# Kernel tuning notes

Measured on AMD Instinct MI355X. Metric: run time of the kernel, lower is better.

## Reference

```python
import jax, jax.numpy as jnp
from jax import lax
import numpy as np

BIG = 1234567891011.0  # sentinel used by the original DTW_TF


def _dtw_cost(D):
    """DTW cost matrix, D: [K,K] pairwise distances -> cost: [K+1,K+1]."""
    K = D.shape[0]
    prev = jnp.concatenate([jnp.zeros((1,), D.dtype), jnp.full((K,), BIG, D.dtype)])  # row 0

    def row_step(prev_row, d_row):
        def col_step(left, vals):
            d, diag, up = vals
            c = d + jnp.minimum(jnp.minimum(left, diag), up)
            return c, c
        _, row_tail = lax.scan(col_step, jnp.asarray(BIG, D.dtype), (d_row, prev_row[:-1], prev_row[1:]))
        row = jnp.concatenate([jnp.full((1,), BIG, D.dtype), row_tail])
        return row, row

    _, rows = lax.scan(row_step, prev, D)
    return jnp.concatenate([prev[None, :], rows], axis=0)


def _dwa_unit(S, W):
    """DTW-aligned 'trace' between window S [K,C] and filter W [K,C].
    Equals trace(gather(S,pi) @ gather(W,pw)^T) = sum over path of dot(S[pi],W[pw])."""
    K = S.shape[0]
    dots = S @ W.T  # [K,K], dots[i,j] = <S[i], W[j]>
    sq = jnp.sum(S * S, axis=1)[:, None] + jnp.sum(W * W, axis=1)[None, :] - 2.0 * dots
    D = jnp.sqrt(jnp.maximum(sq, 0.0))  # euclidean distance matrix
    cost = _dtw_cost(D)  # [K+1,K+1]

    # Backtrack minimal path from (K,K); path has at most 2K-1 kept entries.
    # Original writes (i-1,j-1) each loop iter then drops the last write; the
    # trace is order-independent so we accumulate kept dot-products directly.
    def step(carry, _):
        i, j, acc, active = carry
        cands = jnp.stack([cost[i - 1, j - 1], cost[i, j - 1], cost[i - 1, j]])
        m = jnp.argmin(cands)  # ties -> first, matching tf.argmin
        i2 = i - jnp.where(m == 1, 0, 1)
        j2 = j - jnp.where(m == 2, 0, 1)
        nxt = active & (i2 > 0) & (j2 > 0)  # loop continues -> this write is kept
        acc = acc + jnp.where(nxt, dots[i2 - 1, j2 - 1], 0.0)
        i = jnp.where(active, i2, i)
        j = jnp.where(active, j2, j)
        return (i, j, acc, nxt), None

    init = (jnp.int32(K), jnp.int32(K), dots[K - 1, K - 1], jnp.bool_(True))
    (_, _, acc, _), _ = lax.scan(step, init, None, length=2 * K - 1)
    return acc


def _dwa_cnn(x, w, b):
    K = w.shape[0]
    P = x.shape[1] - K + 1
    Wt = jnp.transpose(w, (2, 0, 1))  # [F,K,C]
    idx = jnp.arange(P)[:, None] + jnp.arange(K)[None, :]  # [P,K]
    windows = x[:, idx, :]  # [B,P,K,C]
    f = jax.vmap(_dwa_unit, in_axes=(None, 0))  # over filters
    f = jax.vmap(f, in_axes=(0, None))          # over positions
    f = jax.vmap(f, in_axes=(0, None))          # over batch
    out = f(windows, Wt)  # [B,P,F]
    return jax.nn.relu(out + b)


def setup_inputs() -> dict:
    key = jax.random.key(0)
    k1, k2 = jax.random.split(key)
    B, T, C, K, F = 32, 2048, 128, 3, 8
    x = jax.random.normal(k1, (B, T, C), dtype=jnp.float32)
    w = jax.random.normal(k2, (K, C, F), dtype=jnp.float32) * 0.1
    b = jnp.zeros((F,), dtype=jnp.float32)
    return {"x": x, "w": w, "b": b}


def reference(x, w, b):
    return _dwa_cnn(x, w, b)
```

## Files before the change

kernel.cpp:

```cpp
#include <hip/hip_runtime.h>


#define TT   62
#define RWS  64
#define DSTR 68

typedef __attribute__((ext_vector_type(8))) short short8v;
typedef __attribute__((ext_vector_type(4))) float f32x4;

static __device__ inline unsigned pk2(float lo, float hi) {
  unsigned r;
  asm("v_cvt_pk_bf16_f32 %0, %1, %2" : "=v"(r) : "v"(lo), "v"(hi));
  return r;
}
static __device__ inline int swzi(int row, int c) {
  return row * 128 + (((c >> 3) ^ (row & 7)) << 3) + (c & 7);
}

static __device__ inline void dpsel(float ca, float cb, float cc,
                                    float Ad, float Al, float Au,
                                    float dist, float dot,
                                    float& costv, float& Av) {
  costv = dist + fminf(fminf(ca, cb), cc);
  const bool d_le_l = (ca <= cb);
  const bool d_le_u = (ca <= cc);
  const bool l_le_u = (cb <= cc);
  Av = dot + (d_le_l ? (d_le_u ? Ad : Au) : (l_le_u ? Al : Au));
}

__global__ __launch_bounds__(256, 4) void dwa_cnn_kernel(
    const float* __restrict__ x, const float* __restrict__ w,
    const float* __restrict__ bias, float* __restrict__ out)
{
  constexpr int T = 2048, C = 128, P = 2046;

  __shared__ alignas(16) unsigned short Wb[32 * 128];
  __shared__ alignas(16) float DsG[RWS * DSTR];
  __shared__ float BI[8];

  const int tid  = threadIdx.x;
  const int b    = blockIdx.y;
  const int p0   = blockIdx.x * TT;
  const int wave = tid >> 6;
  const int lane = tid & 63;
  const int g    = lane >> 4, l15 = lane & 15;
  const int arow = wave * 16 + l15;

  float4 wv[3];
  #pragma unroll
  for (int j = 0; j < 3; ++j)
    wv[j] = *(const float4*)&w[j * 1024 + tid * 4];
  const float breg = (tid < 8) ? bias[tid] : 0.f;

  const float* xr = &x[((size_t)b * T + p0 + arow) * C + g * 8];
  float4 xa[8];
  #pragma unroll
  for (int kk = 0; kk < 4; ++kk) {
    xa[2 * kk]     = *(const float4*)(xr + kk * 32);
    xa[2 * kk + 1] = *(const float4*)(xr + kk * 32 + 4);
  }

  #pragma unroll
  for (int j = 0; j < 3; ++j) {
    const int i4 = j * 1024 + tid * 4;
    const int k = i4 >> 10, c = (i4 >> 3) & 127, f0 = i4 & 7;
    const int q = k * 8 + f0;
    Wb[swzi(q + 0, c)] = (unsigned short)pk2(wv[j].x, wv[j].x);
    Wb[swzi(q + 1, c)] = (unsigned short)pk2(wv[j].y, wv[j].y);
    Wb[swzi(q + 2, c)] = (unsigned short)pk2(wv[j].z, wv[j].z);
    Wb[swzi(q + 3, c)] = (unsigned short)pk2(wv[j].w, wv[j].w);
  }
  { uint2 z = {0u, 0u}; *(uint2*)&Wb[3072 + tid * 4] = z; }
  if (tid < 8) BI[tid] = breg;

  asm volatile("s_waitcnt lgkmcnt(0)\n\ts_barrier" ::: "memory");

  short8v af[4];
  float xn = 0.f;
  #pragma unroll
  for (int kk = 0; kk < 4; ++kk) {
    const float4 a = xa[2 * kk], c4 = xa[2 * kk + 1];
    xn = fmaf(a.x, a.x, fmaf(a.y, a.y, fmaf(a.z, a.z, fmaf(a.w, a.w, xn))));
    xn = fmaf(c4.x, c4.x, fmaf(c4.y, c4.y, fmaf(c4.z, c4.z, fmaf(c4.w, c4.w, xn))));
    uint4 pr;
    pr.x = pk2(a.x, a.y);   pr.y = pk2(a.z, a.w);
    pr.z = pk2(c4.x, c4.y); pr.w = pk2(c4.z, c4.w);
    af[kk] = *(short8v*)&pr;
  }
  xn += __shfl_xor(xn, 16);
  xn += __shfl_xor(xn, 32);

  const int q0 = l15;
  short8v b0f[4], b1f[4];
  #pragma unroll
  for (int kk = 0; kk < 4; ++kk) {
    const int oct = kk * 4 + g;
    b0f[kk] = *(const short8v*)&Wb[swzi(q0,      oct * 8)];
    b1f[kk] = *(const short8v*)&Wb[swzi(q0 + 16, oct * 8)];
  }

  f32x4 acc0 = {0.f, 0.f, 0.f, 0.f}, acc1 = {0.f, 0.f, 0.f, 0.f};
  f32x4 aw0  = {0.f, 0.f, 0.f, 0.f}, aw1  = {0.f, 0.f, 0.f, 0.f};
  #pragma unroll
  for (int kk = 0; kk < 4; ++kk) {
    acc0 = __builtin_amdgcn_mfma_f32_16x16x32_bf16(af[kk], b0f[kk], acc0, 0, 0, 0);
    acc1 = __builtin_amdgcn_mfma_f32_16x16x32_bf16(af[kk], b1f[kk], acc1, 0, 0, 0);
    aw0  = __builtin_amdgcn_mfma_f32_16x16x32_bf16(b0f[kk], b0f[kk], aw0, 0, 0, 0);
    aw1  = __builtin_amdgcn_mfma_f32_16x16x32_bf16(b1f[kk], b1f[kk], aw1, 0, 0, 0);
  }

  float wn0, wn1;
  {
    const int src = ((l15 >> 2) << 4) | l15;
    const int rsel = l15 & 3;
    float s0 = __shfl(aw0[0], src), s1 = __shfl(aw0[1], src);
    float s2 = __shfl(aw0[2], src), s3 = __shfl(aw0[3], src);
    wn0 = (rsel == 0) ? s0 : (rsel == 1) ? s1 : (rsel == 2) ? s2 : s3;
    s0 = __shfl(aw1[0], src); s1 = __shfl(aw1[1], src);
    s2 = __shfl(aw1[2], src); s3 = __shfl(aw1[3], src);
    wn1 = (rsel == 0) ? s0 : (rsel == 1) ? s1 : (rsel == 2) ? s2 : s3;
  }

  {
    const int rq = g * 4;
    #pragma unroll
    for (int r = 0; r < 4; ++r) {
      const float xnv = __shfl(xn, rq + r);
      const int row = wave * 16 + rq + r;
      const float d0 = acc0[r];
      float2 pv0;
      pv0.x = d0;
      pv0.y = sqrtf(fmaxf(xnv + wn0 - 2.f * d0, 0.f));
      *(float2*)&DsG[row * DSTR + q0 * 2] = pv0;
      if (q0 < 8) {
        const float d1 = acc1[r];
        float2 pv1;
        pv1.x = d1;
        pv1.y = sqrtf(fmaxf(xnv + wn1 - 2.f * d1, 0.f));
        *(float2*)&DsG[row * DSTR + (16 + q0) * 2] = pv1;
      }
    }
  }

  asm volatile("s_waitcnt lgkmcnt(0)\n\ts_barrier" ::: "memory");

  if (tid < TT * 4) {
    const int pl = tid >> 2, f0 = (tid & 3) * 2;

    float d0[3][3], s0[3][3], d1[3][3], s1[3][3];
    #pragma unroll
    for (int i = 0; i < 3; ++i) {
      #pragma unroll
      for (int k = 0; k < 3; ++k) {
        const float4 pr = *(const float4*)&DsG[(pl + i) * DSTR + (k * 8 + f0) * 2];
        d0[i][k] = pr.x; s0[i][k] = pr.y;
        d1[i][k] = pr.z; s1[i][k] = pr.w;
      }
    }

    float2 o;
    {
      const float c11 = s0[0][0];
      const float c12 = c11 + s0[0][1];
      const float c13 = c12 + s0[0][2];
      const float c21 = c11 + s0[1][0];
      const float c31 = c21 + s0[2][0];
      const float A11 = d0[0][0];
      const float A12 = A11 + d0[0][1];
      const float A13 = A12 + d0[0][2];
      const float A21 = A11 + d0[1][0];
      const float A31 = A21 + d0[2][0];
      float c22, A22, c23, A23, c32, A32, cxx, A33;
      dpsel(c11, c21, c12, A11, A21, A12, s0[1][1], d0[1][1], c22, A22);
      dpsel(c12, c22, c13, A12, A22, A13, s0[1][2], d0[1][2], c23, A23);
      dpsel(c21, c31, c22, A21, A31, A22, s0[2][1], d0[2][1], c32, A32);
      dpsel(c22, c32, c23, A22, A32, A23, s0[2][2], d0[2][2], cxx, A33);
      o.x = fmaxf(A33 + BI[f0], 0.f);
    }
    {
      const float c11 = s1[0][0];
      const float c12 = c11 + s1[0][1];
      const float c13 = c12 + s1[0][2];
      const float c21 = c11 + s1[1][0];
      const float c31 = c21 + s1[2][0];
      const float A11 = d1[0][0];
      const float A12 = A11 + d1[0][1];
      const float A13 = A12 + d1[0][2];
      const float A21 = A11 + d1[1][0];
      const float A31 = A21 + d1[2][0];
      float c22, A22, c23, A23, c32, A32, cxx, A33;
      dpsel(c11, c21, c12, A11, A21, A12, s1[1][1], d1[1][1], c22, A22);
      dpsel(c12, c22, c13, A12, A22, A13, s1[1][2], d1[1][2], c23, A23);
      dpsel(c21, c31, c22, A21, A31, A22, s1[2][1], d1[2][1], c32, A32);
      dpsel(c22, c32, c23, A22, A32, A23, s1[2][2], d1[2][2], cxx, A33);
      o.y = fmaxf(A33 + BI[f0 + 1], 0.f);
    }

    *(float2*)&out[((size_t)b * P + p0 + pl) * 8 + f0] = o;
  }
}

extern "C" void kernel_launch(void* const* d_in, const int* in_sizes, int n_in,
                              void* d_out, int out_size, void* d_ws, size_t ws_size,
                              hipStream_t stream) {
  const float* x    = (const float*)d_in[0];
  const float* w    = (const float*)d_in[1];
  const float* bias = (const float*)d_in[2];
  float* out        = (float*)d_out;

  dim3 grid(33, 32);
  dwa_cnn_kernel<<<grid, 256, 0, stream>>>(x, w, bias, out);
}
```

Measured before the change: 13.59 us.

## Process two batch elements per block to amortize weight setup

```diff
diff --git a/kernel.cpp b/kernel.cpp
--- a/kernel.cpp
+++ b/kernel.cpp
@@ -28,54 +28,9 @@
   Av = dot + (d_le_l ? (d_le_u ? Ad : Au) : (l_le_u ? Al : Au));
 }
 
-__global__ __launch_bounds__(256, 4) void dwa_cnn_kernel(
-    const float* __restrict__ x, const float* __restrict__ w,
-    const float* __restrict__ bias, float* __restrict__ out)
-{
-  constexpr int T = 2048, C = 128, P = 2046;
-
-  __shared__ alignas(16) unsigned short Wb[32 * 128];
-  __shared__ alignas(16) float DsG[RWS * DSTR];
-  __shared__ float BI[8];
-
-  const int tid  = threadIdx.x;
-  const int b    = blockIdx.y;
-  const int p0   = blockIdx.x * TT;
-  const int wave = tid >> 6;
-  const int lane = tid & 63;
-  const int g    = lane >> 4, l15 = lane & 15;
-  const int arow = wave * 16 + l15;
-
-  float4 wv[3];
-  #pragma unroll
-  for (int j = 0; j < 3; ++j)
-    wv[j] = *(const float4*)&w[j * 1024 + tid * 4];
-  const float breg = (tid < 8) ? bias[tid] : 0.f;
-
-  const float* xr = &x[((size_t)b * T + p0 + arow) * C + g * 8];
-  float4 xa[8];
-  #pragma unroll
-  for (int kk = 0; kk < 4; ++kk) {
-    xa[2 * kk]     = *(const float4*)(xr + kk * 32);
-    xa[2 * kk + 1] = *(const float4*)(xr + kk * 32 + 4);
-  }
-
-  #pragma unroll
-  for (int j = 0; j < 3; ++j) {
-    const int i4 = j * 1024 + tid * 4;
-    const int k = i4 >> 10, c = (i4 >> 3) & 127, f0 = i4 & 7;
-    const int q = k * 8 + f0;
-    Wb[swzi(q + 0, c)] = (unsigned short)pk2(wv[j].x, wv[j].x);
-    Wb[swzi(q + 1, c)] = (unsigned short)pk2(wv[j].y, wv[j].y);
-    Wb[swzi(q + 2, c)] = (unsigned short)pk2(wv[j].z, wv[j].z);
-    Wb[swzi(q + 3, c)] = (unsigned short)pk2(wv[j].w, wv[j].w);
-  }
-  { uint2 z = {0u, 0u}; *(uint2*)&Wb[3072 + tid * 4] = z; }
-  if (tid < 8) BI[tid] = breg;
-
-  asm volatile("s_waitcnt lgkmcnt(0)\n\ts_barrier" ::: "memory");
-
-  short8v af[4];
+#define LGKM_BARRIER() asm volatile("s_waitcnt lgkmcnt(0)\n\ts_barrier" ::: "memory")
+
+static __device__ inline float cvt_frags(const float4* xa, short8v* af) {
   float xn = 0.f;
   #pragma unroll
   for (int kk = 0; kk < 4; ++kk) {
@@ -89,61 +44,33 @@
   }
   xn += __shfl_xor(xn, 16);
   xn += __shfl_xor(xn, 32);
-
-  const int q0 = l15;
-  short8v b0f[4], b1f[4];
-  #pragma unroll
-  for (int kk = 0; kk < 4; ++kk) {
-    const int oct = kk * 4 + g;
-    b0f[kk] = *(const short8v*)&Wb[swzi(q0,      oct * 8)];
-    b1f[kk] = *(const short8v*)&Wb[swzi(q0 + 16, oct * 8)];
-  }
-
-  f32x4 acc0 = {0.f, 0.f, 0.f, 0.f}, acc1 = {0.f, 0.f, 0.f, 0.f};
-  f32x4 aw0  = {0.f, 0.f, 0.f, 0.f}, aw1  = {0.f, 0.f, 0.f, 0.f};
-  #pragma unroll
-  for (int kk = 0; kk < 4; ++kk) {
-    acc0 = __builtin_amdgcn_mfma_f32_16x16x32_bf16(af[kk], b0f[kk], acc0, 0, 0, 0);
-    acc1 = __builtin_amdgcn_mfma_f32_16x16x32_bf16(af[kk], b1f[kk], acc1, 0, 0, 0);
-    aw0  = __builtin_amdgcn_mfma_f32_16x16x32_bf16(b0f[kk], b0f[kk], aw0, 0, 0, 0);
-    aw1  = __builtin_amdgcn_mfma_f32_16x16x32_bf16(b1f[kk], b1f[kk], aw1, 0, 0, 0);
-  }
-
-  float wn0, wn1;
-  {
-    const int src = ((l15 >> 2) << 4) | l15;
-    const int rsel = l15 & 3;
-    float s0 = __shfl(aw0[0], src), s1 = __shfl(aw0[1], src);
-    float s2 = __shfl(aw0[2], src), s3 = __shfl(aw0[3], src);
-    wn0 = (rsel == 0) ? s0 : (rsel == 1) ? s1 : (rsel == 2) ? s2 : s3;
-    s0 = __shfl(aw1[0], src); s1 = __shfl(aw1[1], src);
-    s2 = __shfl(aw1[2], src); s3 = __shfl(aw1[3], src);
-    wn1 = (rsel == 0) ? s0 : (rsel == 1) ? s1 : (rsel == 2) ? s2 : s3;
-  }
-
-  {
-    const int rq = g * 4;
-    #pragma unroll
-    for (int r = 0; r < 4; ++r) {
-      const float xnv = __shfl(xn, rq + r);
-      const int row = wave * 16 + rq + r;
-      const float d0 = acc0[r];
-      float2 pv0;
-      pv0.x = d0;
-      pv0.y = sqrtf(fmaxf(xnv + wn0 - 2.f * d0, 0.f));
-      *(float2*)&DsG[row * DSTR + q0 * 2] = pv0;
-      if (q0 < 8) {
-        const float d1 = acc1[r];
-        float2 pv1;
-        pv1.x = d1;
-        pv1.y = sqrtf(fmaxf(xnv + wn1 - 2.f * d1, 0.f));
-        *(float2*)&DsG[row * DSTR + (16 + q0) * 2] = pv1;
-      }
-    }
-  }
-
-  asm volatile("s_waitcnt lgkmcnt(0)\n\ts_barrier" ::: "memory");
-
+  return xn;
+}
+
+static __device__ inline void write_table(float* DsG, const f32x4& a0, const f32x4& a1,
+                                          float xn, float wn0, float wn1,
+                                          int wave, int g, int q0) {
+  const int rq = g * 4;
+  #pragma unroll
+  for (int r = 0; r < 4; ++r) {
+    const float xnv = __shfl(xn, rq + r);
+    const int row = wave * 16 + rq + r;
+    float2 pv0;
+    pv0.x = a0[r];
+    pv0.y = sqrtf(fmaxf(xnv + wn0 - 2.f * a0[r], 0.f));
+    *(float2*)&DsG[row * DSTR + q0 * 2] = pv0;
+    if (q0 < 8) {
+      float2 pv1;
+      pv1.x = a1[r];
+      pv1.y = sqrtf(fmaxf(xnv + wn1 - 2.f * a1[r], 0.f));
+      *(float2*)&DsG[row * DSTR + (16 + q0) * 2] = pv1;
+    }
+  }
+}
+
+static __device__ inline void dtw_phase2(const float* DsG, const float* BI,
+                                         float* __restrict__ out, int b, int p0,
+                                         int tid) {
   if (tid < TT * 4) {
     const int pl = tid >> 2, f0 = (tid & 3) * 2;
 
@@ -196,8 +123,121 @@
       o.y = fmaxf(A33 + BI[f0 + 1], 0.f);
     }
 
-    *(float2*)&out[((size_t)b * P + p0 + pl) * 8 + f0] = o;
-  }
+    *(float2*)&out[((size_t)b * 2046 + p0 + pl) * 8 + f0] = o;
+  }
+}
+
+__global__ __launch_bounds__(256, 4) void dwa_cnn_kernel(
+    const float* __restrict__ x, const float* __restrict__ w,
+    const float* __restrict__ bias, float* __restrict__ out)
+{
+  constexpr int T = 2048, C = 128;
+
+  __shared__ alignas(16) unsigned short Wb[32 * 128];
+  __shared__ alignas(16) float DsG[RWS * DSTR];
+  __shared__ float BI[8];
+
+  const int tid  = threadIdx.x;
+  const int bq   = blockIdx.y;
+  const int p0   = blockIdx.x * TT;
+  const int wave = tid >> 6;
+  const int lane = tid & 63;
+  const int g    = lane >> 4, l15 = lane & 15;
+  const int arow = wave * 16 + l15;
+
+  float4 wv[3];
+  #pragma unroll
+  for (int j = 0; j < 3; ++j)
+    wv[j] = *(const float4*)&w[j * 1024 + tid * 4];
+  const float breg = (tid < 8) ? bias[tid] : 0.f;
+
+  const float* xr1 = &x[((size_t)bq * T + p0 + arow) * C + g * 8];
+  float4 xa[8];
+  #pragma unroll
+  for (int kk = 0; kk < 4; ++kk) {
+    xa[2 * kk]     = *(const float4*)(xr1 + kk * 32);
+    xa[2 * kk + 1] = *(const float4*)(xr1 + kk * 32 + 4);
+  }
+
+  #pragma unroll
+  for (int j = 0; j < 3; ++j) {
+    const int i4 = j * 1024 + tid * 4;
+    const int k = i4 >> 10, c = (i4 >> 3) & 127, f0 = i4 & 7;
+    const int q = k * 8 + f0;
+    Wb[swzi(q + 0, c)] = (unsigned short)pk2(wv[j].x, wv[j].x);
+    Wb[swzi(q + 1, c)] = (unsigned short)pk2(wv[j].y, wv[j].y);
+    Wb[swzi(q + 2, c)] = (unsigned short)pk2(wv[j].z, wv[j].z);
+    Wb[swzi(q + 3, c)] = (unsigned short)pk2(wv[j].w, wv[j].w);
+  }
+  { uint2 z = {0u, 0u}; *(uint2*)&Wb[3072 + tid * 4] = z; }
+  if (tid < 8) BI[tid] = breg;
+
+  const float* xr2 = &x[(((size_t)bq + 16) * T + p0 + arow) * C + g * 8];
+  float4 xb[8];
+  #pragma unroll
+  for (int kk = 0; kk < 4; ++kk) {
+    xb[2 * kk]     = *(const float4*)(xr2 + kk * 32);
+    xb[2 * kk + 1] = *(const float4*)(xr2 + kk * 32 + 4);
+  }
+
+  LGKM_BARRIER();
+
+  short8v af[4];
+  const float xn1 = cvt_frags(xa, af);
+
+  const int q0 = l15;
+  short8v b0f[4], b1f[4];
+  #pragma unroll
+  for (int kk = 0; kk < 4; ++kk) {
+    const int oct = kk * 4 + g;
+    b0f[kk] = *(const short8v*)&Wb[swzi(q0,      oct * 8)];
+    b1f[kk] = *(const short8v*)&Wb[swzi(q0 + 16, oct * 8)];
+  }
+
+  f32x4 acc0 = {0.f, 0.f, 0.f, 0.f}, acc1 = {0.f, 0.f, 0.f, 0.f};
+  f32x4 aw0  = {0.f, 0.f, 0.f, 0.f}, aw1  = {0.f, 0.f, 0.f, 0.f};
+  #pragma unroll
+  for (int kk = 0; kk < 4; ++kk) {
+    acc0 = __builtin_amdgcn_mfma_f32_16x16x32_bf16(af[kk], b0f[kk], acc0, 0, 0, 0);
+    acc1 = __builtin_amdgcn_mfma_f32_16x16x32_bf16(af[kk], b1f[kk], acc1, 0, 0, 0);
+    aw0  = __builtin_amdgcn_mfma_f32_16x16x32_bf16(b0f[kk], b0f[kk], aw0, 0, 0, 0);
+    aw1  = __builtin_amdgcn_mfma_f32_16x16x32_bf16(b1f[kk], b1f[kk], aw1, 0, 0, 0);
+  }
+
+  float wn0, wn1;
+  {
+    const int src = ((l15 >> 2) << 4) | l15;
+    const int rsel = l15 & 3;
+    float s0 = __shfl(aw0[0], src), s1 = __shfl(aw0[1], src);
+    float s2 = __shfl(aw0[2], src), s3 = __shfl(aw0[3], src);
+    wn0 = (rsel == 0) ? s0 : (rsel == 1) ? s1 : (rsel == 2) ? s2 : s3;
+    s0 = __shfl(aw1[0], src); s1 = __shfl(aw1[1], src);
+    s2 = __shfl(aw1[2], src); s3 = __shfl(aw1[3], src);
+    wn1 = (rsel == 0) ? s0 : (rsel == 1) ? s1 : (rsel == 2) ? s2 : s3;
+  }
+
+  write_table(DsG, acc0, acc1, xn1, wn0, wn1, wave, g, q0);
+
+  LGKM_BARRIER();
+
+  dtw_phase2(DsG, BI, out, bq, p0, tid);
+
+  LGKM_BARRIER();
+
+  short8v af2[4];
+  const float xn2 = cvt_frags(xb, af2);
+  f32x4 e0 = {0.f, 0.f, 0.f, 0.f}, e1 = {0.f, 0.f, 0.f, 0.f};
+  #pragma unroll
+  for (int kk = 0; kk < 4; ++kk) {
+    e0 = __builtin_amdgcn_mfma_f32_16x16x32_bf16(af2[kk], b0f[kk], e0, 0, 0, 0);
+    e1 = __builtin_amdgcn_mfma_f32_16x16x32_bf16(af2[kk], b1f[kk], e1, 0, 0, 0);
+  }
+
+  write_table(DsG, e0, e1, xn2, wn0, wn1, wave, g, q0);
+
+  LGKM_BARRIER();
+
+  dtw_phase2(DsG, BI, out, bq + 16, p0, tid);
 }
 
 extern "C" void kernel_launch(void* const* d_in, const int* in_sizes, int n_in,
@@ -208,6 +248,6 @@
   const float* bias = (const float*)d_in[2];
   float* out        = (float*)d_out;
 
-  dim3 grid(33, 32);
+  dim3 grid(33, 16);
   dwa_cnn_kernel<<<grid, 256, 0, stream>>>(x, w, bias, out);
 }
```

Result: slower. 15.16 us (+11.5%).

## Make each wave self-contained with overlapping row tiles to drop block barrier

Applied to the files above, without the earlier changes.

```diff
diff --git a/kernel.cpp b/kernel.cpp
--- a/kernel.cpp
+++ b/kernel.cpp
@@ -1,9 +1,9 @@
 #include <hip/hip_runtime.h>
 
 
-#define TT   62
-#define RWS  64
-#define DSTR 68
+#define TT    56
+#define WOUT  14
+#define TSTR  52
 
 typedef __attribute__((ext_vector_type(8))) short short8v;
 typedef __attribute__((ext_vector_type(4))) float f32x4;
@@ -35,7 +35,7 @@
   constexpr int T = 2048, C = 128, P = 2046;
 
   __shared__ alignas(16) unsigned short Wb[32 * 128];
-  __shared__ alignas(16) float DsG[RWS * DSTR];
+  __shared__ alignas(16) float TB[4][16 * TSTR];
   __shared__ float BI[8];
 
   const int tid  = threadIdx.x;
@@ -44,7 +44,9 @@
   const int wave = tid >> 6;
   const int lane = tid & 63;
   const int g    = lane >> 4, l15 = lane & 15;
-  const int arow = wave * 16 + l15;
+
+  const int trow0 = p0 + wave * WOUT + l15;
+  const int trow  = (trow0 < T) ? trow0 : (T - 1);
 
   float4 wv[3];
   #pragma unroll
@@ -52,7 +54,7 @@
     wv[j] = *(const float4*)&w[j * 1024 + tid * 4];
   const float breg = (tid < 8) ? bias[tid] : 0.f;
 
-  const float* xr = &x[((size_t)b * T + p0 + arow) * C + g * 8];
+  const float* xr = &x[((size_t)b * T + trow) * C + g * 8];
   float4 xa[8];
   #pragma unroll
   for (int kk = 0; kk < 4; ++kk) {
@@ -121,38 +123,36 @@
     wn1 = (rsel == 0) ? s0 : (rsel == 1) ? s1 : (rsel == 2) ? s2 : s3;
   }
 
+  float* Tw = TB[wave];
   {
     const int rq = g * 4;
     #pragma unroll
     for (int r = 0; r < 4; ++r) {
       const float xnv = __shfl(xn, rq + r);
-      const int row = wave * 16 + rq + r;
-      const float d0 = acc0[r];
+      const int row = rq + r;
       float2 pv0;
-      pv0.x = d0;
-      pv0.y = sqrtf(fmaxf(xnv + wn0 - 2.f * d0, 0.f));
-      *(float2*)&DsG[row * DSTR + q0 * 2] = pv0;
+      pv0.x = acc0[r];
+      pv0.y = sqrtf(fmaxf(xnv + wn0 - 2.f * acc0[r], 0.f));
+      *(float2*)&Tw[row * TSTR + q0 * 2] = pv0;
       if (q0 < 8) {
-        const float d1 = acc1[r];
         float2 pv1;
-        pv1.x = d1;
-        pv1.y = sqrtf(fmaxf(xnv + wn1 - 2.f * d1, 0.f));
-        *(float2*)&DsG[row * DSTR + (16 + q0) * 2] = pv1;
+        pv1.x = acc1[r];
+        pv1.y = sqrtf(fmaxf(xnv + wn1 - 2.f * acc1[r], 0.f));
+        *(float2*)&Tw[row * TSTR + (16 + q0) * 2] = pv1;
       }
     }
   }
 
-  asm volatile("s_waitcnt lgkmcnt(0)\n\ts_barrier" ::: "memory");
-
-  if (tid < TT * 4) {
-    const int pl = tid >> 2, f0 = (tid & 3) * 2;
+  if (lane < WOUT * 4) {
+    const int j = lane >> 2, f0 = (lane & 3) * 2;
+    const int p = p0 + wave * WOUT + j;
 
     float d0[3][3], s0[3][3], d1[3][3], s1[3][3];
     #pragma unroll
     for (int i = 0; i < 3; ++i) {
       #pragma unroll
       for (int k = 0; k < 3; ++k) {
-        const float4 pr = *(const float4*)&DsG[(pl + i) * DSTR + (k * 8 + f0) * 2];
+        const float4 pr = *(const float4*)&Tw[(j + i) * TSTR + (k * 8 + f0) * 2];
         d0[i][k] = pr.x; s0[i][k] = pr.y;
         d1[i][k] = pr.z; s1[i][k] = pr.w;
       }
@@ -196,7 +196,7 @@
       o.y = fmaxf(A33 + BI[f0 + 1], 0.f);
     }
 
-    *(float2*)&out[((size_t)b * P + p0 + pl) * 8 + f0] = o;
+    if (p < P) *(float2*)&out[((size_t)b * P + p) * 8 + f0] = o;
   }
 }
 
@@ -208,6 +208,6 @@
   const float* bias = (const float*)d_in[2];
   float* out        = (float*)d_out;
 
-  dim3 grid(33, 32);
+  dim3 grid(37, 32);
   dwa_cnn_kernel<<<grid, 256, 0, stream>>>(x, w, bias, out);
 }
```

Result: no change. 13.48 us (-0.9%).
